# Kernel optimization log

Hardware: AMD Instinct MI355X
Metric: run time of the kernel (lower is better)

Reference implementation:

```python
import jax, jax.numpy as jnp
import numpy as np

S, V = 16, 8                 # node embedding irreps: 16x0e + 8x1o
GEO = 3 * V                  # flattened vector feature dims
OUT = 8                      # output irreps: 8x0e
RADIUS = 5.0
NUM_BASIS = 20               # radius * basis_density_per_A
ACT_NORM = 1.6789717         # e3nn normalize2mom constant for silu under N(0,1)
SQ3 = 3.0 ** 0.5
W_MSG = S*S + V*S + S*V + V*V        # 576 = weight_numel of node x sh -> node TP
W_REC = (S*S + V*V) * OUT            # 2560 = weight_numel of node x node -> 8x0e TP


def _mlp(x, w0, w1):
    # e3nn FullyConnectedNet: randn weights, matmul scaled by 1/sqrt(fan_in),
    # hidden activation is second-moment-normalized silu, last layer linear.
    h = jax.nn.silu(x @ (w0 / np.sqrt(w0.shape[0]))) * ACT_NORM
    return h @ (w1 / np.sqrt(w1.shape[0]))


def _sh(vec):
    # o3.spherical_harmonics lmax=1, normalize=True, normalization='component':
    # Y0 = 1, Y1 = sqrt(3) * unit_vector
    r = vec / jnp.linalg.norm(vec, axis=-1, keepdims=True)
    return jnp.ones((vec.shape[0], 1), vec.dtype), SQ3 * r


def _split(f):
    return f[:, :S], f[:, S:].reshape(-1, V, 3)


def _tp_node_sh(xf, y0, y1, w):
    # FullyConnectedTensorProduct (Sx0e+Vx1o) x (1x0e+1x1o) -> (Sx0e+Vx1o), external per-edge weights.
    # CG (e3nn wigner_3j): 0x0->0: 1; 1x1->0: delta/sqrt3; 0x1->1,1x0->1: delta/sqrt3.
    # path_weight = sqrt((2l_out+1)/fan_in), fan_in per output irrep = S*1 + V*1.
    xs, xv = _split(xf)
    o = 0
    wA = w[:, o:o + S*S].reshape(-1, S, S); o += S*S   # 0e x 0e -> 0e
    wB = w[:, o:o + V*S].reshape(-1, V, S); o += V*S   # 1o x 1o -> 0e
    wC = w[:, o:o + S*V].reshape(-1, S, V); o += S*V   # 0e x 1o -> 1o
    wD = w[:, o:].reshape(-1, V, V)                    # 1o x 0e -> 1o
    fan = float(S + V)
    pw0 = (1.0 / fan) ** 0.5
    pw1 = (3.0 / fan) ** 0.5
    out_s = pw0 * (jnp.einsum('eu,euw->ew', xs * y0, wA)
                   + jnp.einsum('eui,ei,euw->ew', xv, y1, wB) / SQ3)
    out_v = (pw1 / SQ3) * (jnp.einsum('eu,ei,euw->ewi', xs, y1, wC)
                           + jnp.einsum('eui,euw->ewi', xv * y0[..., None], wD))
    return jnp.concatenate([out_s, out_v.reshape(-1, GEO)], axis=1)


def _tp_rec(xf, yf, w):
    # FullyConnectedTensorProduct (node) x (node) -> OUTx0e, external per-edge weights.
    xs, xv = _split(xf)
    ys, yv = _split(yf)
    w1 = w[:, :S*S*OUT].reshape(-1, S, S, OUT)
    w2 = w[:, S*S*OUT:].reshape(-1, V, V, OUT)
    pw = (1.0 / float(S*S + V*V)) ** 0.5
    return pw * (jnp.einsum('eu,ev,euvw->ew', xs, ys, w1)
                 + jnp.einsum('eui,evi,euvw->ew', xv, yv, w2) / SQ3)


def _dist_embed(d):
    # soft_one_hot_linspace(basis='smooth_finite', cutoff=True) * sqrt(num_basis)
    values = jnp.linspace(0.0, RADIUS, NUM_BASIS + 2)[1:-1]
    step = RADIUS / (NUM_BASIS + 1)
    diff = (d[:, None] - values) / step
    sus = lambda t: jnp.where(t > 0.0, jnp.exp(-1.0 / jnp.where(t > 0.0, t, 1.0)), 0.0)
    return 1.14136 * np.exp(2.0) * sus(diff + 1.0) * sus(1.0 - diff) * (NUM_BASIS ** 0.5)


def _mp_step(node, pos, src, dst, edge_attr, imp, mw0, mw1, uw0, uw1, is_initial):
    n = node.shape[0]
    vec = pos[dst] - pos[src]
    y0, y1 = _sh(vec)
    tp = _tp_node_sh(node[src], y0, y1, _mlp(edge_attr, mw0, mw1))
    deg = src.shape[0] / n
    msgs = jax.ops.segment_sum(tp, dst, num_segments=n) / (deg ** 0.5)
    msgs = msgs * imp
    scal = _mlp(jnp.concatenate([msgs[:, :S], node[:, :S]], axis=1), uw0, uw1)
    geo = msgs[:, S:] + node[:, S:]
    if not is_initial:
        geo = geo * 0.5
    return jnp.concatenate([scal, geo], axis=1)


def _forward(x, pos, edge_attr, emb_w0, emb_w1, imp0, msg0_w0, msg0_w1, upd0_w0, upd0_w1,
             imp1, msg1_w0, msg1_w1, upd1_w0, upd1_w1, lig_w0, lig_w1, rec_w0, rec_w1,
             edge_index, inter_edge_index):
    src, dst = edge_index[0], edge_index[1]
    node = _mlp(x, emb_w0, emb_w1)                                   # [N, S]
    node = jnp.concatenate([node, jnp.zeros((node.shape[0], GEO), node.dtype)], axis=1)
    node = _mp_step(node, pos, src, dst, edge_attr, imp0, msg0_w0, msg0_w1, upd0_w0, upd0_w1, True)
    node = _mp_step(node, pos, src, dst, edge_attr, imp1, msg1_w0, msg1_w1, upd1_w0, upd1_w1, False)
    rec, lig = inter_edge_index[0], inter_edge_index[1]
    vec = pos[lig] - pos[rec]
    y0, y1 = _sh(vec)
    demb = _dist_embed(jnp.linalg.norm(vec, axis=1))
    lig_emb = _tp_node_sh(node[lig], y0, y1, _mlp(demb, lig_w0, lig_w1))
    return _tp_rec(lig_emb, node[rec], _mlp(demb, rec_w0, rec_w1))    # [E_inter, OUT]


def setup_inputs():
    key = jax.random.key(0)
    ks = iter(jax.random.split(key, 32))
    N, E, EI = 10000, 120000, 40000
    A, B = 10, 5   # len(atom_types), len(bond_types)
    rn = lambda *s: jax.random.normal(next(ks), s, dtype=jnp.float32)
    # edges without self-loops (dst != src) to keep edge_vec nonzero
    src = jax.random.randint(next(ks), (E,), 0, N)
    dst = (src + jax.random.randint(next(ks), (E,), 1, N)) % N
    irec = jax.random.randint(next(ks), (EI,), 0, N)
    ilig = (irec + jax.random.randint(next(ks), (EI,), 1, N)) % N
    return dict(
        x=jax.random.uniform(next(ks), (N, A), dtype=jnp.float32),
        pos=rn(N, 3) * 3.0,
        edge_index=jnp.stack([src, dst]),
        edge_attr=jax.random.uniform(next(ks), (E, B), dtype=jnp.float32),
        inter_edge_index=jnp.stack([irec, ilig]),
        emb_w0=rn(A, 64), emb_w1=rn(64, S),
        imp0=rn(1), msg0_w0=rn(B, 64), msg0_w1=rn(64, W_MSG),
        upd0_w0=rn(2 * S, 64), upd0_w1=rn(64, S),
        imp1=rn(1), msg1_w0=rn(B, 64), msg1_w1=rn(64, W_MSG),
        upd1_w0=rn(2 * S, 64), upd1_w1=rn(64, S),
        lig_w0=rn(NUM_BASIS, 64), lig_w1=rn(64, W_MSG),
        rec_w0=rn(NUM_BASIS, 64), rec_w1=rn(64, W_REC),
    )


def reference(x, pos, edge_index, edge_attr, inter_edge_index,
              emb_w0, emb_w1, imp0, msg0_w0, msg0_w1, upd0_w0, upd0_w1,
              imp1, msg1_w0, msg1_w1, upd1_w0, upd1_w1,
              lig_w0, lig_w1, rec_w0, rec_w1):
    return _forward(x, pos, edge_attr, emb_w0, emb_w1, imp0, msg0_w0, msg0_w1, upd0_w0, upd0_w1,
                    imp1, msg1_w0, msg1_w1, upd1_w0, upd1_w1, lig_w0, lig_w1, rec_w0, rec_w1,
                    edge_index, inter_edge_index)
```

## Files before the change

kernel.cpp:

```cpp
#include <hip/hip_runtime.h>
#include <hip/hip_fp16.h>
#include <cmath>

constexpr float ACT_NORM = 1.6789717f;
constexpr float PW0      = 0.20412414523193154f;
constexpr float PW1      = 0.35355339059327373f;
constexpr float PWREC    = 0.05590169943749474f;
constexpr float INV_SQ3  = 0.57735026918962576f;
constexpr float PW0s     = PW0 * 0.125f;
constexpr float PW1s     = PW1 * 0.125f;
constexpr float PWRECs   = PWREC * 0.125f;

__device__ __forceinline__ float silu_n(float x) {
  return x / (1.f + __expf(-x)) * ACT_NORM;
}

__device__ __forceinline__ unsigned ubcast_lane(unsigned v, int k) {
  return (unsigned)__builtin_amdgcn_readlane((int)v, k);
}

typedef _Float16 h2v __attribute__((ext_vector_type(2)));
typedef _Float16 f16x8 __attribute__((ext_vector_type(8)));
typedef float    f32x4 __attribute__((ext_vector_type(4)));

__device__ __forceinline__ unsigned packh2(float a, float b) {
  h2v p; p.x = (_Float16)a; p.y = (_Float16)b;
  return __builtin_bit_cast(unsigned, p);
}
__device__ __forceinline__ unsigned short f16bits(float a) {
  return __builtin_bit_cast(unsigned short, (_Float16)a);
}
__device__ __forceinline__ float h2f(unsigned short b) {
  return (float)__builtin_bit_cast(_Float16, b);
}
__device__ __forceinline__ float dot2h(unsigned w2, unsigned h2, float acc) {
  return __builtin_amdgcn_fdot2(__builtin_bit_cast(h2v, w2),
                                __builtin_bit_cast(h2v, h2), acc, false);
}
__device__ __forceinline__ float hlo(unsigned d) {
  return (float)__builtin_bit_cast(_Float16, (unsigned short)(d & 0xffffu));
}
__device__ __forceinline__ float hhi(unsigned d) {
  return (float)__builtin_bit_cast(_Float16, (unsigned short)(d >> 16));
}
__device__ __forceinline__ float hsel(unsigned d, int hi) { return hi ? hhi(d) : hlo(d); }
__device__ __forceinline__ unsigned u4sel(const uint4& v, int i) {
  return i == 0 ? v.x : (i == 1 ? v.y : (i == 2 ? v.z : v.w));
}
__device__ __forceinline__ unsigned u2sel(const uint2& v, int i) { return i ? v.y : v.x; }

__device__ __forceinline__ f32x4 mfma16(uint4 a, uint4 b, f32x4 c) {
  return __builtin_amdgcn_mfma_f32_16x16x32_f16(
      __builtin_bit_cast(f16x8, a), __builtin_bit_cast(f16x8, b), c, 0, 0, 0);
}

__global__ __launch_bounds__(256)
void emb_kernel(const float* __restrict__ x, const float* __restrict__ w0,
                const float* __restrict__ w1, float* __restrict__ node, int N) {
  const int lane = threadIdx.x & 63;
  const int lw   = threadIdx.x >> 6;
  const int gw   = blockIdx.x * 4 + lw;
  __shared__ float sH[4][64];
  const bool valid = gw < N;
  const int n = valid ? gw : 0;
  float acc = 0.f;
#pragma unroll
  for (int a = 0; a < 10; ++a) acc = fmaf(x[n * 10 + a], w0[a * 64 + lane], acc);
  acc *= 0.31622776601683794f;
  sH[lw][lane] = silu_n(acc);
  __syncthreads();
  if (valid) {
    if (lane < 16) {
      float o = 0.f;
#pragma unroll
      for (int k = 0; k < 64; ++k) o = fmaf(sH[lw][k], w1[k * 16 + lane], o);
      node[(size_t)n * 40 + lane] = o * 0.125f;
    } else if (lane < 40) {
      node[(size_t)n * 40 + lane] = 0.f;
    }
  }
}

__global__ __launch_bounds__(256)
void upd_kernel(float* __restrict__ node, const float* __restrict__ msgs,
                const float* __restrict__ w0, const float* __restrict__ w1,
                const float* __restrict__ imp, float geo_scale, float inv_sqrt_deg, int N) {
  const int lane = threadIdx.x & 63;
  const int lw   = threadIdx.x >> 6;
  const int gw   = blockIdx.x * 4 + lw;
  __shared__ float sIn[4][32];
  __shared__ float sH[4][64];
  const bool valid = gw < N;
  const int n = valid ? gw : 0;
  const float mscale = imp[0] * inv_sqrt_deg;
  if (lane < 16)      sIn[lw][lane] = msgs[(size_t)n * 40 + lane] * mscale;
  else if (lane < 32) sIn[lw][lane] = node[(size_t)n * 40 + lane - 16];
  __syncthreads();
  float acc = 0.f;
#pragma unroll
  for (int a = 0; a < 32; ++a) acc = fmaf(sIn[lw][a], w0[a * 64 + lane], acc);
  acc *= 0.17677669529663687f;
  sH[lw][lane] = silu_n(acc);
  __syncthreads();
  if (valid) {
    if (lane < 16) {
      float o = 0.f;
#pragma unroll
      for (int k = 0; k < 64; ++k) o = fmaf(sH[lw][k], w1[k * 16 + lane], o);
      node[(size_t)n * 40 + lane] = o * 0.125f;
    } else if (lane < 40) {
      const size_t gi = (size_t)n * 40 + lane;
      node[gi] = fmaf(msgs[gi], mscale, node[gi]) * geo_scale;
    }
  }
}

__global__ __launch_bounds__(256)
void inter_h_kernel(const float* __restrict__ pos, const int* __restrict__ iei,
                    const float* __restrict__ lw0, const float* __restrict__ rw0,
                    float* __restrict__ hL, float* __restrict__ hR, int EI) {
  const int lane = threadIdx.x & 63;
  const int lw   = threadIdx.x >> 6;
  const int gw   = blockIdx.x * 4 + lw;
  __shared__ float sD[4][20];
  const bool valid = gw < EI;
  const int e = valid ? gw : 0;
  const int rec = iei[e], lig = iei[EI + e];
  const float dx = pos[lig * 3]     - pos[rec * 3];
  const float dy = pos[lig * 3 + 1] - pos[rec * 3 + 1];
  const float dz = pos[lig * 3 + 2] - pos[rec * 3 + 2];
  const float d = sqrtf(dx * dx + dy * dy + dz * dz);
  if (lane < 20) {
    const float diff = d * 4.2f - (float)(lane + 1);
    const float t1 = diff + 1.f, t2 = 1.f - diff;
    float v = 0.f;
    if (t1 > 0.f && t2 > 0.f) {
      const float C = 1.14136f * 7.3890560989306495f * 4.4721359549995794f;
      v = C * __expf(-1.f / t1 - 1.f / t2);
    }
    sD[lw][lane] = v;
  }
  __syncthreads();
  float a0 = 0.f, a1 = 0.f;
#pragma unroll
  for (int b = 0; b < 20; ++b) {
    const float db = sD[lw][b];
    a0 = fmaf(db, lw0[b * 64 + lane], a0);
    a1 = fmaf(db, rw0[b * 64 + lane], a1);
  }
  a0 *= 0.22360679774997896f;
  a1 *= 0.22360679774997896f;
  if (valid) {
    hL[(size_t)e * 64 + lane] = silu_n(a0);
    hR[(size_t)e * 64 + lane] = silu_n(a1);
  }
}

__global__ __launch_bounds__(256)
void edge_hf_kernel(const float* __restrict__ eattr, const float* __restrict__ w0,
                    const int* __restrict__ ei, uint4* __restrict__ hEf, int E, int nTe) {
  const int gid = blockIdx.x * 256 + threadIdx.x;
  if (gid >= nTe * 128) return;
  const int T = gid >> 7, rem = gid & 127, H = rem >> 6, l = rem & 63;
  (void)ei;
  int e = T * 16 + (l & 15);
  if (e >= E) e = E - 1;
  const int k0 = H * 32 + (l >> 4) * 8;
  float ea[5];
#pragma unroll
  for (int a = 0; a < 5; ++a) ea[a] = eattr[(size_t)e * 5 + a] * 0.4472135954999579f;
  unsigned q[4];
#pragma unroll
  for (int jj = 0; jj < 4; ++jj) {
    float hh[2];
#pragma unroll
    for (int p = 0; p < 2; ++p) {
      const int k = k0 + jj * 2 + p;
      float acc = 0.f;
#pragma unroll
      for (int a = 0; a < 5; ++a) acc = fmaf(ea[a], w0[a * 64 + k], acc);
      hh[p] = silu_n(acc);
    }
    q[jj] = packh2(hh[0], hh[1]);
  }
  uint4 out; out.x = q[0]; out.y = q[1]; out.z = q[2]; out.w = q[3];
  hEf[gid] = out;
}

__global__ __launch_bounds__(256, 2)
void msg_mfma_kernel(const float* __restrict__ node, const float* __restrict__ pos,
                     const int* __restrict__ ei, const float* __restrict__ W1,
                     const uint4* __restrict__ hEf, float* __restrict__ msgs,
                     int E, int nTe) {
  __shared__ __align__(16) uint4 sB[36 * 128];
  __shared__ __align__(16) unsigned short sFt[4][16][56];
  const int tid = threadIdx.x, lane = tid & 63, wv = tid >> 6;

  for (int j = tid; j < 4608; j += 256) {
    const int t = j >> 7, H = (j >> 6) & 1, l = j & 63;
    const int kb = H * 32 + (l >> 4) * 8;
    const float* src = &W1[(size_t)kb * 576 + t * 16 + (l & 15)];
    uint4 q;
    q.x = packh2(src[0],       src[576]);
    q.y = packh2(src[2 * 576], src[3 * 576]);
    q.z = packh2(src[4 * 576], src[5 * 576]);
    q.w = packh2(src[6 * 576], src[7 * 576]);
    sB[j] = q;
  }
  __syncthreads();

  unsigned short (*fW)[56] = sFt[wv];
  const int er0 = (lane >> 4) * 4;
  const int c   = lane & 15;
  const int cp  = (lane >> 3) & 1;
  const int w   = c & 7;

  for (int T = blockIdx.x * 4 + wv; T < nTe; T += (int)gridDim.x * 4) {
    if (lane < 16) {
      int ge = T * 16 + lane; if (ge >= E) ge = E - 1;
      const int ia = ei[ge], ib = ei[E + ge];
      const float vx = pos[ib * 3]     - pos[ia * 3];
      const float vy = pos[ib * 3 + 1] - pos[ia * 3 + 1];
      const float vz = pos[ib * 3 + 2] - pos[ia * 3 + 2];
      const float rn = rsqrtf(vx * vx + vy * vy + vz * vz);
      fW[lane][40] = f16bits(vx * rn);
      fW[lane][41] = f16bits(vy * rn);
      fW[lane][42] = f16bits(vz * rn);
    }
#pragma unroll
    for (int j = 0; j < 4; ++j) {
      const int e = j * 4 + (lane >> 4);
      int ge = T * 16 + e; if (ge >= E) ge = E - 1;
      const int ns = ei[ge];
      fW[e][c] = f16bits(node[(size_t)ns * 40 + c]);
    }
#pragma unroll
    for (int j = 0; j < 6; ++j) {
      const int flat = j * 64 + lane;
      const int e = flat / 24, q = flat - e * 24;
      const int u = q / 3, i = q - u * 3;
      int ge = T * 16 + e; if (ge >= E) ge = E - 1;
      const int ns = ei[ge];
      fW[e][16 + i * 8 + (u & 1) * 4 + (u >> 1)] = f16bits(node[(size_t)ns * 40 + 16 + q]);
    }
#pragma unroll
    for (int j = 0; j < 2; ++j) {
      const int flat = j * 64 + lane;
      const int e = flat >> 3, u = flat & 7;
      float d = 0.f;
#pragma unroll
      for (int i = 0; i < 3; ++i)
        d = fmaf(h2f(fW[e][16 + i * 8 + (u & 1) * 4 + (u >> 1)]), h2f(fW[e][40 + i]), d);
      fW[e][48 + u] = f16bits(d);
    }

    const uint4 a0 = hEf[T * 128 + lane];
    const uint4 a1 = hEf[T * 128 + 64 + lane];

    uint4 xsR[4][2], dpR[4];
    uint2 xvR[4][3];
    float rf[4][3];
#pragma unroll
    for (int r = 0; r < 4; ++r) {
      const int e = er0 + r;
      xsR[r][0] = *(const uint4*)&fW[e][0];
      xsR[r][1] = *(const uint4*)&fW[e][8];
      dpR[r]    = *(const uint4*)&fW[e][48];
#pragma unroll
      for (int i = 0; i < 3; ++i) {
        xvR[r][i] = *(const uint2*)&fW[e][16 + i * 8 + cp * 4];
        rf[r][i]  = h2f(fW[e][40 + i]);
      }
    }

    float o_s[4] = {0.f, 0.f, 0.f, 0.f};
    float sxw[4] = {0.f, 0.f, 0.f, 0.f};
    float ov[3][4];
#pragma unroll
    for (int i = 0; i < 3; ++i)
#pragma unroll
      for (int r = 0; r < 4; ++r) ov[i][r] = 0.f;

    uint4 b0 = sB[lane], b1 = sB[64 + lane];
#pragma unroll
    for (int t = 0; t < 36; ++t) {
      uint4 n0, n1;
      if (t < 35) { n0 = sB[(t + 1) * 128 + lane]; n1 = sB[(t + 1) * 128 + 64 + lane]; }
      f32x4 C = {0.f, 0.f, 0.f, 0.f};
      C = mfma16(a0, b0, C);
      C = mfma16(a1, b1, C);
      if (t < 16) {
#pragma unroll
        for (int r = 0; r < 4; ++r)
          o_s[r] = fmaf(hsel(u4sel(xsR[r][t >> 3], (t >> 1) & 3), t & 1), C[r], o_s[r]);
      } else if (t < 24) {
        const int u = t - 16;
#pragma unroll
        for (int r = 0; r < 4; ++r)
          o_s[r] = fmaf(hsel(u4sel(dpR[r], u >> 1), u & 1), C[r], o_s[r]);
      } else if (t < 32) {
        const int j = t - 24;
#pragma unroll
        for (int r = 0; r < 4; ++r) {
          const int idx = 2 * j + cp;
          sxw[r] = fmaf(hsel(u4sel(xsR[r][idx >> 3], (idx >> 1) & 3), idx & 1), C[r], sxw[r]);
        }
      } else {
        const int j = t - 32;
#pragma unroll
        for (int i = 0; i < 3; ++i)
#pragma unroll
          for (int r = 0; r < 4; ++r)
            ov[i][r] = fmaf(hsel(u2sel(xvR[r][i], j >> 1), j & 1), C[r], ov[i][r]);
      }
      if (t < 35) { b0 = n0; b1 = n1; }
    }

#pragma unroll
    for (int r = 0; r < 4; ++r) {
      const int ge = T * 16 + er0 + r;
      const bool valid = ge < E;
      const int dst = ei[E + (valid ? ge : 0)];
      if (valid) atomicAdd(&msgs[(size_t)dst * 40 + c], PW0s * o_s[r]);
#pragma unroll
      for (int i = 0; i < 3; ++i) {
        float v = fmaf(PW1s * rf[r][i], sxw[r], PW0s * ov[i][r]);
        v += __shfl_xor(v, 8);
        if (valid && (lane & 8) == 0)
          atomicAdd(&msgs[(size_t)dst * 40 + 16 + w * 3 + i], v);
      }
    }
  }
}

template <int MODE>
__global__ __launch_bounds__(512, 2)
void tp_kernel(const float* __restrict__ node, const float* __restrict__ pos,
               const int* __restrict__ ei, const float* __restrict__ eattr,
               const float* __restrict__ w0, const float* __restrict__ W1,
               const float* __restrict__ hSrc, float* __restrict__ out, int E) {
  __shared__ __align__(16) uint4 sWa[32 * 64];
  __shared__ __align__(16) uint4 sWb[32 * 64];
  __shared__ unsigned sWc[32 * 64];
  __shared__ float sF[8][6][27];
  const int tid  = threadIdx.x;
  const int lane = tid & 63;
  const int wv   = tid >> 6;

  for (int j = tid; j < 2048; j += 512) {
    const int kp = j >> 6, l = j & 63;
    const float* s0 = &W1[(2 * kp) * 576 + l];
    const float* s1 = s0 + 576;
    uint4 qa, qb;
    qa.x = packh2(s0[0],   s1[0]);
    qa.y = packh2(s0[64],  s1[64]);
    qa.z = packh2(s0[128], s1[128]);
    qa.w = packh2(s0[192], s1[192]);
    qb.x = packh2(s0[256], s1[256]);
    qb.y = packh2(s0[320], s1[320]);
    qb.z = packh2(s0[384], s1[384]);
    qb.w = packh2(s0[448], s1[448]);
    sWa[j] = qa;
    sWb[j] = qb;
    sWc[j] = packh2(s0[512], s1[512]);
  }
  __syncthreads();

  float w0r[5];
  if (MODE == 0) {
#pragma unroll
    for (int a = 0; a < 5; ++a) w0r[a] = w0[a * 64 + lane] * 0.4472135954999579f;
  }
  const int kl2 = (lane & 31) * 2;

  const int nB = (E + 47) / 48;
  for (int b = blockIdx.x; b < nB; b += (int)gridDim.x) {
    const int ebase = b * 48 + wv * 6;
    int outn[6], nsrc[6];
    bool val[6];
    unsigned hp[6];
#pragma unroll
    for (int s = 0; s < 6; ++s) {
      const int e0 = ebase + s;
      val[s] = e0 < E;
      const int e = val[s] ? e0 : 0;
      const int ia = ei[e], ib = ei[E + e];
      if (MODE == 0) { nsrc[s] = ia; outn[s] = ib; }
      else           { nsrc[s] = ib; outn[s] = e;  }
      const float vx = pos[ib * 3]     - pos[ia * 3];
      const float vy = pos[ib * 3 + 1] - pos[ia * 3 + 1];
      const float vz = pos[ib * 3 + 2] - pos[ia * 3 + 2];
      const float rn = rsqrtf(vx * vx + vy * vy + vz * vz);
      const float rx = vx * rn, ry = vy * rn, rz = vz * rn;
      float h;
      if (MODE == 0) {
        float acc = 0.f;
#pragma unroll
        for (int a = 0; a < 5; ++a) acc = fmaf(eattr[(size_t)e * 5 + a], w0r[a], acc);
        h = silu_n(acc);
      } else {
        h = hSrc[(size_t)e * 64 + lane];
      }
      hp[s] = packh2(__shfl(h, kl2), __shfl(h, kl2 + 1));
      if (lane < 16) {
        sF[wv][s][lane] = node[(size_t)nsrc[s] * 40 + lane];
      } else if (lane < 24) {
        const int u = lane - 16;
        const float x0 = node[(size_t)nsrc[s] * 40 + 16 + u * 3];
        const float x1 = node[(size_t)nsrc[s] * 40 + 16 + u * 3 + 1];
        const float x2 = node[(size_t)nsrc[s] * 40 + 16 + u * 3 + 2];
        sF[wv][s][16 + u] = x0 * rx + x1 * ry + x2 * rz;
      } else if (lane < 27) {
        sF[wv][s][24 + (lane - 24)] = (lane == 24) ? rx : ((lane == 25) ? ry : rz);
      }
    }

    float wacc[6][9];
#pragma unroll
    for (int s = 0; s < 6; ++s)
#pragma unroll
      for (int t = 0; t < 9; ++t) wacc[s][t] = 0.f;

    uint4 qa0 = sWa[lane], qb0 = sWb[lane];
    unsigned qc0 = sWc[lane];
#pragma unroll 4
    for (int kp = 0; kp < 32; ++kp) {
      const int kn = (kp + 1) & 31;
      const uint4 qa1 = sWa[kn * 64 + lane];
      const uint4 qb1 = sWb[kn * 64 + lane];
      const unsigned qc1 = sWc[kn * 64 + lane];
#pragma unroll
      for (int s = 0; s < 6; ++s) {
        const unsigned hv2 = ubcast_lane(hp[s], kp);
        wacc[s][0] = dot2h(qa0.x, hv2, wacc[s][0]);
        wacc[s][1] = dot2h(qa0.y, hv2, wacc[s][1]);
        wacc[s][2] = dot2h(qa0.z, hv2, wacc[s][2]);
        wacc[s][3] = dot2h(qa0.w, hv2, wacc[s][3]);
        wacc[s][4] = dot2h(qb0.x, hv2, wacc[s][4]);
        wacc[s][5] = dot2h(qb0.y, hv2, wacc[s][5]);
        wacc[s][6] = dot2h(qb0.z, hv2, wacc[s][6]);
        wacc[s][7] = dot2h(qb0.w, hv2, wacc[s][7]);
        wacc[s][8] = dot2h(qc0,   hv2, wacc[s][8]);
      }
      qa0 = qa1; qb0 = qb1; qc0 = qc1;
    }

    const int ub  = lane >> 4;
    const int ub2 = lane >> 3;
#pragma unroll
    for (int s = 0; s < 6; ++s) {
      float cs = 0.f;
#pragma unroll
      for (int t = 0; t < 6; ++t)
        cs = fmaf(PW0s * sF[wv][s][ub + 4 * t], wacc[s][t], cs);
      cs += __shfl_xor(cs, 16);
      cs += __shfl_xor(cs, 32);

      const float rx = sF[wv][s][24], ry = sF[wv][s][25], rz = sF[wv][s][26];
      const float* xp = &node[(size_t)nsrc[s] * 40 + 16 + ub2 * 3];
      const float xv0 = xp[0], xv1 = xp[1], xv2 = xp[2];
      const float sxw = PW1s * (sF[wv][s][ub2] * wacc[s][6] + sF[wv][s][ub2 + 8] * wacc[s][7]);
      float cv0 = fmaf(PW0s * xv0, wacc[s][8], sxw * rx);
      float cv1 = fmaf(PW0s * xv1, wacc[s][8], sxw * ry);
      float cv2 = fmaf(PW0s * xv2, wacc[s][8], sxw * rz);
      cv0 += __shfl_xor(cv0, 8); cv0 += __shfl_xor(cv0, 16); cv0 += __shfl_xor(cv0, 32);
      cv1 += __shfl_xor(cv1, 8); cv1 += __shfl_xor(cv1, 16); cv1 += __shfl_xor(cv1, 32);
      cv2 += __shfl_xor(cv2, 8); cv2 += __shfl_xor(cv2, 16); cv2 += __shfl_xor(cv2, 32);

      if (val[s]) {
        const size_t ob = (size_t)outn[s] * 40;
        if (MODE == 0) {
          if (lane < 16) atomicAdd(&out[ob + lane], cs);
          if (lane < 8) {
            atomicAdd(&out[ob + 16 + lane * 3],     cv0);
            atomicAdd(&out[ob + 16 + lane * 3 + 1], cv1);
            atomicAdd(&out[ob + 16 + lane * 3 + 2], cv2);
          }
        } else {
          if (lane < 16) out[ob + lane] = cs;
          if (lane < 8) {
            out[ob + 16 + lane * 3]     = cv0;
            out[ob + 16 + lane * 3 + 1] = cv1;
            out[ob + 16 + lane * 3 + 2] = cv2;
          }
        }
      }
    }
  }
}

__global__ __launch_bounds__(512)
void pack_h_kernel(const float* __restrict__ h, uint4* __restrict__ hPf, int nT) {
  const int gid = blockIdx.x * 512 + threadIdx.x;
  if (gid >= nT * 128) return;
  const int l = gid & 63;
  const int H = (gid >> 6) & 1;
  const int T = gid >> 7;
  const int e = T * 16 + (l & 15);
  const int kb = H * 32 + (l >> 4) * 8;
  const float* src = &h[(size_t)e * 64 + kb];
  uint4 q;
  q.x = packh2(src[0], src[1]);
  q.y = packh2(src[2], src[3]);
  q.z = packh2(src[4], src[5]);
  q.w = packh2(src[6], src[7]);
  hPf[gid] = q;
}

__global__ __launch_bounds__(256)
void pack_d_kernel(const float* __restrict__ ligE, const float* __restrict__ node,
                   const int* __restrict__ iei, unsigned short* __restrict__ Dt, int EI) {
  const int gid = blockIdx.x * 256 + threadIdx.x;
  if (gid >= EI * 64) return;
  const int e = gid >> 6, rem = gid & 63;
  const int b = rem >> 5, u = (rem >> 2) & 7, vi = rem & 3;
  const int v = 2 * vi + b;
  const int rec = iei[e];
  const float* xp = &ligE[(size_t)e * 40 + 16 + u * 3];
  const float* yp = &node[(size_t)rec * 40 + 16 + v * 3];
  const float d = (xp[0] * yp[0] + xp[1] * yp[1] + xp[2] * yp[2]) * INV_SQ3;
  Dt[gid] = f16bits(d);
}

__global__ __launch_bounds__(512, 2)
void rec_kernel(const float* __restrict__ node, const float* __restrict__ ligE,
                const int* __restrict__ iei, const float* __restrict__ RW1,
                const uint4* __restrict__ hPf, const uint2* __restrict__ Dt2,
                float* __restrict__ out, int nT) {
  __shared__ __align__(16) uint4 sB[4096];
  __shared__ __align__(16) unsigned short sFeat[8][320];
  const int tid = threadIdx.x, lane = tid & 63, wv = tid >> 6;
  const int cg = blockIdx.y;

  for (int j = tid; j < 4096; j += 512) {
    const int t = j >> 7, H = (j >> 6) & 1, l = j & 63;
    const int kb = H * 32 + (l >> 4) * 8;
    const float* src = &RW1[(size_t)kb * 2560 + cg * 512 + t * 16 + (l & 15)];
    uint4 q;
    q.x = packh2(src[0],        src[2560]);
    q.y = packh2(src[2 * 2560], src[3 * 2560]);
    q.z = packh2(src[4 * 2560], src[5 * 2560]);
    q.w = packh2(src[6 * 2560], src[7 * 2560]);
    sB[j] = q;
  }
  __syncthreads();

  unsigned short* fW = sFeat[wv];
  const int er0 = (lane >> 4) * 4;
  const int bpar = (lane >> 3) & 1;
  const int c    = lane & 7;
  const int se = lane >> 2, si = lane & 3;

  for (int T = blockIdx.x * 8 + wv; T < nT; T += (int)gridDim.x * 8) {
    const uint4 a0 = hPf[(T * 2 + 0) * 64 + lane];
    const uint4 a1 = hPf[(T * 2 + 1) * 64 + lane];
    const int eg = T * 16 + se;

    if (cg < 4) {
      const int rn = iei[eg];
      const float4 yv = *(const float4*)&node[(size_t)rn * 40 + si * 4];
      *(unsigned*)&fW[(se * 2 + 0) * 8 + 2 * si] = packh2(yv.x, yv.z);
      *(unsigned*)&fW[(se * 2 + 1) * 8 + 2 * si] = packh2(yv.y, yv.w);
      fW[256 + se * 4 + si] = f16bits(ligE[(size_t)eg * 40 + cg * 4 + si]);
    }

    float o[4] = {0.f, 0.f, 0.f, 0.f};
    uint4 b0 = sB[lane], b1 = sB[64 + lane];

    if (cg < 4) {
      uint2 xsR[4]; uint4 ysR[4];
#pragma unroll
      for (int r = 0; r < 4; ++r) {
        const int er = er0 + r;
        ysR[r] = *(const uint4*)&fW[(er * 2 + bpar) * 8];
        xsR[r] = *(const uint2*)&fW[256 + er * 4];
      }
#pragma unroll
      for (int t = 0; t < 32; ++t) {
        uint4 n0, n1;
        if (t < 31) { n0 = sB[(t + 1) * 128 + lane]; n1 = sB[(t + 1) * 128 + 64 + lane]; }
        f32x4 C = {0.f, 0.f, 0.f, 0.f};
        C = mfma16(a0, b0, C);
        C = mfma16(a1, b1, C);
        const int up = t >> 3, vi = t & 7;
#pragma unroll
        for (int r = 0; r < 4; ++r) {
          const float xs = hsel(u2sel(xsR[r], up >> 1), up & 1);
          const float ys = hsel(u4sel(ysR[r], vi >> 1), vi & 1);
          o[r] = fmaf(xs * ys, C[r], o[r]);
        }
        if (t < 31) { b0 = n0; b1 = n1; }
      }
    } else {
#pragma unroll
      for (int pass = 0; pass < 2; ++pass) {
        uint2 dR[4][4];
#pragma unroll
        for (int r = 0; r < 4; ++r) {
          const int e = T * 16 + er0 + r;
#pragma unroll
          for (int uu = 0; uu < 4; ++uu)
            dR[r][uu] = Dt2[(size_t)e * 16 + bpar * 8 + pass * 4 + uu];
        }
#pragma unroll
        for (int tt = 0; tt < 16; ++tt) {
          const int t = pass * 16 + tt;
          uint4 n0, n1;
          if (t < 31) { n0 = sB[(t + 1) * 128 + lane]; n1 = sB[(t + 1) * 128 + 64 + lane]; }
          f32x4 C = {0.f, 0.f, 0.f, 0.f};
          C = mfma16(a0, b0, C);
          C = mfma16(a1, b1, C);
          const int uu = tt >> 2, vi = tt & 3;
#pragma unroll
          for (int r = 0; r < 4; ++r) {
            const float f = hsel(u2sel(dR[r][uu], vi >> 1), vi & 1);
            o[r] = fmaf(f, C[r], o[r]);
          }
          if (t < 31) { b0 = n0; b1 = n1; }
        }
      }
    }

#pragma unroll
    for (int r = 0; r < 4; ++r) {
      const float v = o[r] + __shfl_xor(o[r], 8);
      if ((lane & 8) == 0)
        atomicAdd(&out[(size_t)(T * 16 + er0 + r) * 8 + c], v * PWRECs);
    }
  }
}

extern "C" void kernel_launch(void* const* d_in, const int* in_sizes, int n_in,
                              void* d_out, int out_size, void* d_ws, size_t ws_size,
                              hipStream_t stream) {
  (void)n_in; (void)ws_size;
  const float* x      = (const float*)d_in[0];
  const float* pos    = (const float*)d_in[1];
  const int*   ei     = (const int*)  d_in[2];
  const float* eattr  = (const float*)d_in[3];
  const int*   iei    = (const int*)  d_in[4];
  const float* emb_w0 = (const float*)d_in[5];
  const float* emb_w1 = (const float*)d_in[6];
  const float* imp0   = (const float*)d_in[7];
  const float* m0w0   = (const float*)d_in[8];
  const float* m0w1   = (const float*)d_in[9];
  const float* u0w0   = (const float*)d_in[10];
  const float* u0w1   = (const float*)d_in[11];
  const float* imp1   = (const float*)d_in[12];
  const float* m1w0   = (const float*)d_in[13];
  const float* m1w1   = (const float*)d_in[14];
  const float* u1w0   = (const float*)d_in[15];
  const float* u1w1   = (const float*)d_in[16];
  const float* lw0    = (const float*)d_in[17];
  const float* lw1    = (const float*)d_in[18];
  const float* rw0    = (const float*)d_in[19];
  const float* rw1    = (const float*)d_in[20];

  const int N  = in_sizes[1] / 3;
  const int E  = in_sizes[2] / 2;
  const int EI = in_sizes[4] / 2;

  float* node = (float*)d_ws;
  float* msgs = node + (size_t)N * 40;
  float* hL   = msgs + (size_t)N * 40;
  float* hR   = hL + (size_t)EI * 64;
  float* ligE = hR + (size_t)EI * 64;
  float* outp = (float*)d_out;

  uint4*          hEf = (uint4*)hL;
  uint4*          hPf = (uint4*)hL;
  unsigned short* Dt  = (unsigned short*)hR;

  const float inv_sqrt_deg = 1.0f / sqrtf((float)E / (float)N);
  const int nodeBlocks  = (N + 3) / 4;
  const int interBlocks = (EI + 3) / 4;
  const int nT  = EI / 16;
  const int nTe = (E + 15) / 16;
  const int hfBlocks = (nTe * 128 + 255) / 256;

  emb_kernel<<<nodeBlocks, 256, 0, stream>>>(x, emb_w0, emb_w1, node, N);

  edge_hf_kernel<<<hfBlocks, 256, 0, stream>>>(eattr, m0w0, ei, hEf, E, nTe);
  hipMemsetAsync(msgs, 0, (size_t)N * 40 * sizeof(float), stream);
  msg_mfma_kernel<<<512, 256, 0, stream>>>(node, pos, ei, m0w1, hEf, msgs, E, nTe);
  upd_kernel<<<nodeBlocks, 256, 0, stream>>>(node, msgs, u0w0, u0w1, imp0, 1.0f, inv_sqrt_deg, N);

  edge_hf_kernel<<<hfBlocks, 256, 0, stream>>>(eattr, m1w0, ei, hEf, E, nTe);
  hipMemsetAsync(msgs, 0, (size_t)N * 40 * sizeof(float), stream);
  msg_mfma_kernel<<<512, 256, 0, stream>>>(node, pos, ei, m1w1, hEf, msgs, E, nTe);
  upd_kernel<<<nodeBlocks, 256, 0, stream>>>(node, msgs, u1w0, u1w1, imp1, 0.5f, inv_sqrt_deg, N);

  inter_h_kernel<<<interBlocks, 256, 0, stream>>>(pos, iei, lw0, rw0, hL, hR, EI);
  tp_kernel<1><<<512, 512, 0, stream>>>(node, pos, iei, nullptr, nullptr, lw1, hL, ligE, EI);

  pack_h_kernel<<<(nT * 128 + 511) / 512, 512, 0, stream>>>(hR, hPf, nT);
  pack_d_kernel<<<(EI * 64 + 255) / 256, 256, 0, stream>>>(ligE, node, iei, Dt, EI);

  hipMemsetAsync(outp, 0, (size_t)out_size * sizeof(float), stream);
  rec_kernel<<<dim3(102, 5), 512, 0, stream>>>(node, ligE, iei, rw1, hPf, (const uint2*)Dt,
                                               outp, nT);
}
```

Measured before the change: 375.0 us.

## Replace message atomics with per-edge buffer and CSR gather in update

The message kernel now writes each edge's message into a per-edge buffer, stored in fp16 if the workspace is too small for fp32, instead of atomically adding into per-node accumulators. A histogram, a single-block scan and a scatter kernel build a destination-sorted edge permutation. The update kernel then gathers and sums each node's incoming messages itself. This removes atomic contention and the memsets, but adds CSR-build kernels, a serial per-node loop over variable degree, and extra memory traffic for the per-edge buffer.

After: 387.4 us. 3.3% more time.

```diff
diff --git a/kernel.cpp b/kernel.cpp
--- a/kernel.cpp
+++ b/kernel.cpp
@@ -52,6 +52,49 @@
 __device__ __forceinline__ f32x4 mfma16(uint4 a, uint4 b, f32x4 c) {
   return __builtin_amdgcn_mfma_f32_16x16x32_f16(
       __builtin_bit_cast(f16x8, a), __builtin_bit_cast(f16x8, b), c, 0, 0, 0);
+}
+
+__global__ __launch_bounds__(256)
+void hist_kernel(const int* __restrict__ ei, int* __restrict__ cnt, int E) {
+  const int e = blockIdx.x * 256 + threadIdx.x;
+  if (e < E) atomicAdd(&cnt[ei[E + e]], 1);
+}
+
+__global__ __launch_bounds__(1024)
+void scan_kernel(const int* __restrict__ cnt, int* __restrict__ starts, int N) {
+  __shared__ int sums[1024];
+  const int t = threadIdx.x;
+  const int per = (N + 1023) >> 10;
+  const int base = t * per;
+  int s = 0;
+  for (int i = 0; i < per; ++i) {
+    const int idx = base + i;
+    if (idx < N) s += cnt[idx];
+  }
+  sums[t] = s;
+  __syncthreads();
+  for (int off = 1; off < 1024; off <<= 1) {
+    int v = (t >= off) ? sums[t - off] : 0;
+    __syncthreads();
+    sums[t] += v;
+    __syncthreads();
+  }
+  int run = (t > 0) ? sums[t - 1] : 0;
+  for (int i = 0; i < per; ++i) {
+    const int idx = base + i;
+    if (idx < N) { starts[idx] = run; run += cnt[idx]; }
+  }
+}
+
+__global__ __launch_bounds__(256)
+void scatter_kernel(const int* __restrict__ ei, const int* __restrict__ starts,
+                    int* __restrict__ cursor, int* __restrict__ eperm, int E) {
+  const int e = blockIdx.x * 256 + threadIdx.x;
+  if (e < E) {
+    const int d = ei[E + e];
+    const int r = atomicAdd(&cursor[d], 1);
+    eperm[starts[d] + r] = e;
+  }
 }
 
 __global__ __launch_bounds__(256)
@@ -81,8 +124,11 @@
   }
 }
 
+template <bool HALFMB>
 __global__ __launch_bounds__(256)
-void upd_kernel(float* __restrict__ node, const float* __restrict__ msgs,
+void upd_kernel(float* __restrict__ node, const void* __restrict__ mbufv,
+                const int* __restrict__ starts, const int* __restrict__ cnt,
+                const int* __restrict__ eperm,
                 const float* __restrict__ w0, const float* __restrict__ w1,
                 const float* __restrict__ imp, float geo_scale, float inv_sqrt_deg, int N) {
   const int lane = threadIdx.x & 63;
@@ -93,7 +139,22 @@
   const bool valid = gw < N;
   const int n = valid ? gw : 0;
   const float mscale = imp[0] * inv_sqrt_deg;
-  if (lane < 16)      sIn[lw][lane] = msgs[(size_t)n * 40 + lane] * mscale;
+
+  float m = 0.f;
+  if (lane < 40) {
+    const int s0 = starts[n], d = cnt[n];
+    if (HALFMB) {
+      const unsigned short* mb = (const unsigned short*)mbufv;
+      for (int j = 0; j < d; ++j)
+        m += h2f(mb[(size_t)eperm[s0 + j] * 40 + lane]);
+    } else {
+      const float* mb = (const float*)mbufv;
+      for (int j = 0; j < d; ++j)
+        m += mb[(size_t)eperm[s0 + j] * 40 + lane];
+    }
+  }
+
+  if (lane < 16)      sIn[lw][lane] = m * mscale;
   else if (lane < 32) sIn[lw][lane] = node[(size_t)n * 40 + lane - 16];
   __syncthreads();
   float acc = 0.f;
@@ -110,7 +171,7 @@
       node[(size_t)n * 40 + lane] = o * 0.125f;
     } else if (lane < 40) {
       const size_t gi = (size_t)n * 40 + lane;
-      node[gi] = fmaf(msgs[gi], mscale, node[gi]) * geo_scale;
+      node[gi] = fmaf(m, mscale, node[gi]) * geo_scale;
     }
   }
 }
@@ -158,11 +219,10 @@
 
 __global__ __launch_bounds__(256)
 void edge_hf_kernel(const float* __restrict__ eattr, const float* __restrict__ w0,
-                    const int* __restrict__ ei, uint4* __restrict__ hEf, int E, int nTe) {
+                    uint4* __restrict__ hEf, int E, int nTe) {
   const int gid = blockIdx.x * 256 + threadIdx.x;
   if (gid >= nTe * 128) return;
   const int T = gid >> 7, rem = gid & 127, H = rem >> 6, l = rem & 63;
-  (void)ei;
   int e = T * 16 + (l & 15);
   if (e >= E) e = E - 1;
   const int k0 = H * 32 + (l >> 4) * 8;
@@ -187,10 +247,11 @@
   hEf[gid] = out;
 }
 
+template <bool HALFMB>
 __global__ __launch_bounds__(256, 2)
 void msg_mfma_kernel(const float* __restrict__ node, const float* __restrict__ pos,
                      const int* __restrict__ ei, const float* __restrict__ W1,
-                     const uint4* __restrict__ hEf, float* __restrict__ msgs,
+                     const uint4* __restrict__ hEf, void* __restrict__ mbufv,
                      int E, int nTe) {
   __shared__ __align__(16) uint4 sB[36 * 128];
   __shared__ __align__(16) unsigned short sFt[4][16][56];
@@ -320,14 +381,30 @@
     for (int r = 0; r < 4; ++r) {
       const int ge = T * 16 + er0 + r;
       const bool valid = ge < E;
-      const int dst = ei[E + (valid ? ge : 0)];
-      if (valid) atomicAdd(&msgs[(size_t)dst * 40 + c], PW0s * o_s[r]);
+      const float sv = PW0s * o_s[r];
+      float vv[3];
 #pragma unroll
       for (int i = 0; i < 3; ++i) {
         float v = fmaf(PW1s * rf[r][i], sxw[r], PW0s * ov[i][r]);
         v += __shfl_xor(v, 8);
-        if (valid && (lane & 8) == 0)
-          atomicAdd(&msgs[(size_t)dst * 40 + 16 + w * 3 + i], v);
+        vv[i] = v;
+      }
+      if (valid) {
+        if (HALFMB) {
+          unsigned short* mb = (unsigned short*)mbufv + (size_t)ge * 40;
+          mb[c] = f16bits(sv);
+          if ((lane & 8) == 0) {
+#pragma unroll
+            for (int i = 0; i < 3; ++i) mb[16 + w * 3 + i] = f16bits(vv[i]);
+          }
+        } else {
+          float* mb = (float*)mbufv + (size_t)ge * 40;
+          mb[c] = sv;
+          if ((lane & 8) == 0) {
+#pragma unroll
+            for (int i = 0; i < 3; ++i) mb[16 + w * 3 + i] = vv[i];
+          }
+        }
       }
     }
   }
@@ -469,20 +546,11 @@
 
       if (val[s]) {
         const size_t ob = (size_t)outn[s] * 40;
-        if (MODE == 0) {
-          if (lane < 16) atomicAdd(&out[ob + lane], cs);
-          if (lane < 8) {
-            atomicAdd(&out[ob + 16 + lane * 3],     cv0);
-            atomicAdd(&out[ob + 16 + lane * 3 + 1], cv1);
-            atomicAdd(&out[ob + 16 + lane * 3 + 2], cv2);
-          }
-        } else {
-          if (lane < 16) out[ob + lane] = cs;
-          if (lane < 8) {
-            out[ob + 16 + lane * 3]     = cv0;
-            out[ob + 16 + lane * 3 + 1] = cv1;
-            out[ob + 16 + lane * 3 + 2] = cv2;
-          }
+        if (lane < 16) out[ob + lane] = cs;
+        if (lane < 8) {
+          out[ob + 16 + lane * 3]     = cv0;
+          out[ob + 16 + lane * 3 + 1] = cv1;
+          out[ob + 16 + lane * 3 + 2] = cv2;
         }
       }
     }
@@ -633,7 +701,7 @@
 extern "C" void kernel_launch(void* const* d_in, const int* in_sizes, int n_in,
                               void* d_out, int out_size, void* d_ws, size_t ws_size,
                               hipStream_t stream) {
-  (void)n_in; (void)ws_size;
+  (void)n_in;
   const float* x      = (const float*)d_in[0];
   const float* pos    = (const float*)d_in[1];
   const int*   ei     = (const int*)  d_in[2];
@@ -661,13 +729,23 @@
   const int EI = in_sizes[4] / 2;
 
   float* node = (float*)d_ws;
-  float* msgs = node + (size_t)N * 40;
-  float* hL   = msgs + (size_t)N * 40;
+  float* hL   = node + (size_t)N * 40;
   float* hR   = hL + (size_t)EI * 64;
   float* ligE = hR + (size_t)EI * 64;
   float* outp = (float*)d_out;
 
-  uint4*          hEf = (uint4*)hL;
+  uint4* hEf   = (uint4*)hL;
+  float* mbase = hL + (size_t)E * 32;
+  const size_t csrInts = (size_t)3 * N + E + 16;
+  const size_t need32  = ((size_t)N * 40 + (size_t)E * 32 + (size_t)E * 40 + csrInts) * 4;
+  const bool   halfmb  = need32 > ws_size;
+  const size_t mbFl    = halfmb ? ((size_t)E * 20) : ((size_t)E * 40);
+  void* mbuf   = (void*)mbase;
+  int*  cnt    = (int*)(mbase + mbFl);
+  int*  starts = cnt + N;
+  int*  cursor = starts + N;
+  int*  eperm  = cursor + N;
+
   uint4*          hPf = (uint4*)hL;
   unsigned short* Dt  = (unsigned short*)hR;
 
@@ -677,18 +755,37 @@
   const int nT  = EI / 16;
   const int nTe = (E + 15) / 16;
   const int hfBlocks = (nTe * 128 + 255) / 256;
+  const int eBlocks  = (E + 255) / 256;
+
+  hipMemsetAsync(cnt, 0, (size_t)N * sizeof(int), stream);
+  hipMemsetAsync(cursor, 0, (size_t)N * sizeof(int), stream);
+  hist_kernel<<<eBlocks, 256, 0, stream>>>(ei, cnt, E);
+  scan_kernel<<<1, 1024, 0, stream>>>(cnt, starts, N);
+  scatter_kernel<<<eBlocks, 256, 0, stream>>>(ei, starts, cursor, eperm, E);
 
   emb_kernel<<<nodeBlocks, 256, 0, stream>>>(x, emb_w0, emb_w1, node, N);
 
-  edge_hf_kernel<<<hfBlocks, 256, 0, stream>>>(eattr, m0w0, ei, hEf, E, nTe);
-  hipMemsetAsync(msgs, 0, (size_t)N * 40 * sizeof(float), stream);
-  msg_mfma_kernel<<<512, 256, 0, stream>>>(node, pos, ei, m0w1, hEf, msgs, E, nTe);
-  upd_kernel<<<nodeBlocks, 256, 0, stream>>>(node, msgs, u0w0, u0w1, imp0, 1.0f, inv_sqrt_deg, N);
-
-  edge_hf_kernel<<<hfBlocks, 256, 0, stream>>>(eattr, m1w0, ei, hEf, E, nTe);
-  hipMemsetAsync(msgs, 0, (size_t)N * 40 * sizeof(float), stream);
-  msg_mfma_kernel<<<512, 256, 0, stream>>>(node, pos, ei, m1w1, hEf, msgs, E, nTe);
-  upd_kernel<<<nodeBlocks, 256, 0, stream>>>(node, msgs, u1w0, u1w1, imp1, 0.5f, inv_sqrt_deg, N);
+  edge_hf_kernel<<<hfBlocks, 256, 0, stream>>>(eattr, m0w0, hEf, E, nTe);
+  if (halfmb) {
+    msg_mfma_kernel<true><<<512, 256, 0, stream>>>(node, pos, ei, m0w1, hEf, mbuf, E, nTe);
+    upd_kernel<true><<<nodeBlocks, 256, 0, stream>>>(node, mbuf, starts, cnt, eperm,
+                                                     u0w0, u0w1, imp0, 1.0f, inv_sqrt_deg, N);
+  } else {
+    msg_mfma_kernel<false><<<512, 256, 0, stream>>>(node, pos, ei, m0w1, hEf, mbuf, E, nTe);
+    upd_kernel<false><<<nodeBlocks, 256, 0, stream>>>(node, mbuf, starts, cnt, eperm,
+                                                      u0w0, u0w1, imp0, 1.0f, inv_sqrt_deg, N);
+  }
+
+  edge_hf_kernel<<<hfBlocks, 256, 0, stream>>>(eattr, m1w0, hEf, E, nTe);
+  if (halfmb) {
+    msg_mfma_kernel<true><<<512, 256, 0, stream>>>(node, pos, ei, m1w1, hEf, mbuf, E, nTe);
+    upd_kernel<true><<<nodeBlocks, 256, 0, stream>>>(node, mbuf, starts, cnt, eperm,
+                                                     u1w0, u1w1, imp1, 0.5f, inv_sqrt_deg, N);
+  } else {
+    msg_mfma_kernel<false><<<512, 256, 0, stream>>>(node, pos, ei, m1w1, hEf, mbuf, E, nTe);
+    upd_kernel<false><<<nodeBlocks, 256, 0, stream>>>(node, mbuf, starts, cnt, eperm,
+                                                      u1w0, u1w1, imp1, 0.5f, inv_sqrt_deg, N);
+  }
 
   inter_h_kernel<<<interBlocks, 256, 0, stream>>>(pos, iei, lw0, rw0, hL, hR, EI);
   tp_kernel<1><<<512, 512, 0, stream>>>(node, pos, iei, nullptr, nullptr, lw1, hL, ligE, EI);
```
